# Performance work log

Hardware: AMD Instinct MI355X
Metric: run time of the kernel (lower is better)

Reference implementation:

```python
import jax, jax.numpy as jnp
import numpy as np

N_NODES = 50000
N_RELS = 50
N_CLASSES = 10
EMB = 16
RP = 16
NT = 300000
EPS = 1e-6


def setup_inputs() -> dict:
    key = jax.random.key(0)
    ks = jax.random.split(key, 8)
    # unique (s, o) pairs of the relational graph
    s = jax.random.randint(ks[0], (NT,), 0, N_NODES, dtype=jnp.int32)
    o = jax.random.randint(ks[1], (NT,), 0, N_NODES, dtype=jnp.int32)
    rm = jnp.arange(RP, dtype=jnp.int32)[:, None]  # (rp, 1)
    # hindices = [s, o*rm] in an (n, n*rp) matrix; vindices = [s*rm, o] in (n*rp, n)
    hrow = jnp.broadcast_to(s[None, :], (RP, NT)).reshape(-1)
    hcol = (o[None, :] * rm).reshape(-1)
    vrow = (s[None, :] * rm).reshape(-1)
    vcol = jnp.broadcast_to(o[None, :], (RP, NT)).reshape(-1)
    # nhots: one-hot relation indicator per unique pair
    p = jax.random.randint(ks[2], (NT,), 0, N_RELS)
    nhots = jnp.zeros((NT, N_RELS), jnp.float32).at[jnp.arange(NT), p].set(1.0)
    # to_latent MLPs (ldepth=0 -> single Linear)
    Wl1 = jax.random.normal(ks[3], (N_RELS, RP), jnp.float32) * 0.1
    bl1 = jnp.zeros((RP,), jnp.float32)
    Wl2 = jax.random.normal(ks[4], (N_RELS, RP), jnp.float32) * 0.1
    bl2 = jnp.zeros((RP,), jnp.float32)
    # xavier-uniform-ish init with relu gain
    g1 = np.sqrt(2.0) * np.sqrt(6.0 / (N_NODES + EMB))
    g2 = np.sqrt(2.0) * np.sqrt(6.0 / (EMB + N_CLASSES))
    weights1 = jax.random.uniform(ks[5], (RP, N_NODES, EMB), jnp.float32, -g1, g1)
    weights2 = jax.random.uniform(ks[6], (RP, EMB, N_CLASSES), jnp.float32, -g2, g2)
    bias1 = jnp.zeros((EMB,), jnp.float32)
    bias2 = jnp.zeros((N_CLASSES,), jnp.float32)
    return {
        "nhots": nhots, "hrow": hrow, "hcol": hcol, "vrow": vrow, "vcol": vcol,
        "Wl1": Wl1, "bl1": bl1, "Wl2": Wl2, "bl2": bl2,
        "weights1": weights1, "bias1": bias1, "weights2": weights2, "bias2": bias2,
    }


def reference(nhots, hrow, hcol, vrow, vcol, Wl1, bl1, Wl2, bl2,
              weights1, bias1, weights2, bias2):
    rp, n, e = weights1.shape
    c = weights2.shape[2]
    # --- layer 1: latent relation mixing over horizontal sparse pattern ---
    lat1 = jax.nn.softmax(nhots @ Wl1 + bl1, axis=1)      # (nt, rp)
    lat1 = lat1.T.reshape(-1)                              # (rp*nt,) value per nnz
    # sum_sparse with row=False: normalize by column sums of the (n, n*rp) matrix
    colsum = jax.ops.segment_sum(lat1, hcol, num_segments=n * rp)
    lat1 = lat1 / jnp.clip(colsum[hcol], EPS, None)
    # spmm: (n, n*rp) sparse @ weights1.view(n*rp, e)
    Xw = weights1.reshape(rp * n, e)
    h = jax.ops.segment_sum(lat1[:, None] * Xw[hcol], hrow, num_segments=n)  # (n, e)
    h = jax.nn.relu(h + bias1)
    # --- layer 2: vertical sparse pattern ---
    lat2 = jax.nn.softmax(nhots @ Wl2 + bl2, axis=1)      # (nt, rp)
    lat2 = jax.nn.relu(lat2.T.reshape(-1))                 # LACT = relu
    # sum_sparse with row=True: normalize by row sums of the (n*rp, n) matrix
    rowsum = jax.ops.segment_sum(lat2, vrow, num_segments=n * rp)
    lat2 = lat2 / jnp.clip(rowsum[vrow], EPS, None)
    # spmm: (n*rp, n) sparse @ h
    h2 = jax.ops.segment_sum(lat2[:, None] * h[vcol], vrow, num_segments=n * rp)  # (n*rp, e)
    h2 = h2.reshape(rp, n, e)
    logits = jnp.einsum('rhc,rnh->nc', weights2, h2) + bias2  # (n, c)
    return logits
```

## Files before the change

### kernel.cpp

```cpp
#include <hip/hip_runtime.h>
#include <hip/hip_bf16.h>
#include <stdint.h>

#define NTOT  300000
#define NNODE 50000
#define RPD   16
#define NREL  50
#define EMB   16
#define NC    10
#define EPSF  1e-6f
#define SG    49

typedef const __hip_bfloat16* bf16p;

__device__ __forceinline__ float b2f(__hip_bfloat16 x){ return __bfloat162float(x); }

__device__ __forceinline__ void unpack2(unsigned u, float& a, float& b){
  a = __uint_as_float(u << 16);
  b = __uint_as_float(u & 0xffff0000u);
}

__device__ __forceinline__ float ldf(const void* p, int i, int bf){
  return bf ? b2f(((bf16p)p)[i]) : ((const float*)p)[i];
}

__global__ void k_detect(const unsigned* nraw, int* flag){
  __shared__ int bad;
  if(threadIdx.x == 0) bad = 0;
  __syncthreads();
  for(int i = threadIdx.x; i < 4096; i += 1024){
    unsigned w = nraw[i];
    if(w != 0u && w != 0x3F800000u) bad = 1;
  }
  __syncthreads();
  if(threadIdx.x == 0) *flag = bad;
}

__global__ void k_zero(float* p, long n){
  long i = (long)blockIdx.x*blockDim.x + threadIdx.x;
  long stride = (long)gridDim.x*blockDim.x;
  for(; i < n; i += stride) p[i] = 0.f;
}

__global__ void k_tables(const void* Wl1, const void* bl1, const void* Wl2, const void* bl2,
                         float* T1, float* T2, const int* flag){
  int bf = *flag;
  int i = threadIdx.x;
  const void* W = nullptr; const void* bl = nullptr; float* T = nullptr; int row = -1;
  if(i < NREL){ W = Wl1; bl = bl1; T = T1; row = i; }
  else if(i >= 64 && i < 64 + NREL){ W = Wl2; bl = bl2; T = T2; row = i - 64; }
  if(row >= 0){
    float v[RPD]; float m = -1e30f;
    for(int r = 0; r < RPD; r++){
      v[r] = ldf(W, row*RPD + r, bf) + ldf(bl, r, bf);
      m = fmaxf(m, v[r]);
    }
    float s = 0.f;
    for(int r = 0; r < RPD; r++){ v[r] = __expf(v[r] - m); s += v[r]; }
    float inv = 1.f / s;
    for(int r = 0; r < RPD; r++) T[row*RPD + r] = v[r] * inv;
  }
}

__global__ __launch_bounds__(256) void k_argmax(const void* nhots, const int* srow, const int* ocol,
    int* p, int* cnt_s, int* cnt_o, const int* flag){
  int bf = *flag;
  int t = blockIdx.x*256 + threadIdx.x;
  if(t >= NTOT) return;
  int pt = 0; float best = -1e30f;
  if(bf){
    const unsigned* row = (const unsigned*)nhots + (size_t)t*(NREL/2);
    for(int k = 0; k < NREL/2; k++){
      float a, b; unpack2(row[k], a, b);
      if(a > best){ best = a; pt = 2*k;   }
      if(b > best){ best = b; pt = 2*k+1; }
    }
  } else {
    const uint2* row = (const uint2*)((const float*)nhots + (size_t)t*NREL);
    for(int k = 0; k < NREL/2; k++){
      uint2 u = row[k];
      float a = __uint_as_float(u.x), b = __uint_as_float(u.y);
      if(a > best){ best = a; pt = 2*k;   }
      if(b > best){ best = b; pt = 2*k+1; }
    }
  }
  p[t] = pt;
  atomicAdd(&cnt_s[srow[t]], 1);
  atomicAdd(&cnt_o[ocol[t]], 1);
}

__global__ __launch_bounds__(1024) void k_scanA(const int* cnt_s, const int* cnt_o,
    int* start_s, int* start_o, int* bsum){
  int G = gridDim.x >> 1;
  bool oside = blockIdx.x >= G;
  int b = oside ? blockIdx.x - G : blockIdx.x;
  const int* cnt = oside ? cnt_o : cnt_s;
  int* start = oside ? start_o : start_s;
  __shared__ int sh[1024];
  int tid = threadIdx.x;
  int idx = b*1024 + tid;
  int v = (idx < NNODE) ? cnt[idx] : 0;
  sh[tid] = v;
  __syncthreads();
  for(int off = 1; off < 1024; off <<= 1){
    int n = (tid >= off) ? sh[tid - off] : 0;
    __syncthreads();
    sh[tid] += n;
    __syncthreads();
  }
  if(idx < NNODE) start[idx] = sh[tid] - v;
  if(tid == 1023) bsum[(oside ? G : 0) + b] = sh[1023];
}

__global__ void k_scanB(int* bsum, int* start_s, int* start_o){
  int tid = threadIdx.x;
  bool oside = tid >= 64;
  int lane = tid & 63;
  int base = oside ? SG : 0;
  int v = (lane < SG) ? bsum[base + lane] : 0;
  int orig = v;
  for(int off = 1; off < 64; off <<= 1){
    int n = __shfl_up(v, off);
    if(lane >= off) v += n;
  }
  if(lane < SG) bsum[base + lane] = v - orig;
  if(lane == 63){
    if(oside) start_o[NNODE] = v; else start_s[NNODE] = v;
  }
}

__global__ __launch_bounds__(1024) void k_scanC(int* start_s, int* start_o,
    int* cursor_s, int* cursor_o, const int* bsum){
  int G = gridDim.x >> 1;
  bool oside = blockIdx.x >= G;
  int b = oside ? blockIdx.x - G : blockIdx.x;
  int idx = b*1024 + threadIdx.x;
  if(idx >= NNODE) return;
  int ofs = bsum[(oside ? G : 0) + b];
  int* start  = oside ? start_o  : start_s;
  int* cursor = oside ? cursor_o : cursor_s;
  int v = start[idx] + ofs;
  start[idx] = v;
  cursor[idx] = v;
}

__global__ void k_fill2(const int* srow, const int* ocol, int* cursor_s, int* cursor_o,
                        int* eidx_s, int* pos_s, int* eidx_o){
  int half = gridDim.x >> 1;
  bool oside = blockIdx.x >= half;
  int b = oside ? blockIdx.x - half : blockIdx.x;
  int t = b*256 + threadIdx.x;
  if(t >= NTOT) return;
  if(oside){ int pos = atomicAdd(&cursor_o[ocol[t]], 1); eidx_o[pos] = t; }
  else     { int pos = atomicAdd(&cursor_s[srow[t]], 1); eidx_s[pos] = t; pos_s[t] = pos; }
}

__global__ __launch_bounds__(256) void k_S12(const int* start_s, const int* eidx_s,
    const int* start_o, const int* eidx_o, const int* p, const float* T1, const float* T2,
    float* S1, float* S2, float* floodS){
  int G = gridDim.x >> 1;
  bool oside = blockIdx.x >= G;
  int b = oside ? blockIdx.x - G : blockIdx.x;
  const int* start = oside ? start_o : start_s;
  const int* eidx  = oside ? eidx_o  : eidx_s;
  const float* T   = oside ? T1 : T2;
  float* S         = oside ? S1 : S2;
  __shared__ float lT[NREL*RPD];
  __shared__ float w0[4];
  int tid = threadIdx.x;
  for(int i = tid; i < NREL*RPD; i += 256) lT[i] = T[i];
  __syncthreads();
  int wave = tid >> 6, lane = tid & 63;
  int r = lane & 15, quarter = lane >> 4;
  float flood = 0.f;
  for(int node = b*4 + wave; node < NNODE; node += G*4){
    float acc = 0.f;
    int e0 = start[node], e1 = start[node+1];
    for(int e = e0 + quarter; e < e1; e += 4)
      acc += lT[p[eidx[e]]*RPD + r];
    acc += __shfl_xor(acc, 16);
    acc += __shfl_xor(acc, 32);
    if(quarter == 0){
      S[node*RPD + r] = acc;
      if(r == 0) flood += acc;
    }
  }
  if(lane == 0) w0[wave] = flood;
  __syncthreads();
  if(tid == 0)
    atomicAdd(&floodS[(oside ? 0 : 64) + (b & 63)], w0[0]+w0[1]+w0[2]+w0[3]);
}

__global__ __launch_bounds__(256) void k_icolsum(const float* S1, const float* floodS, float* icolsum){
  int stride = gridDim.x*256;
  for(int v = blockIdx.x*256 + threadIdx.x; v < NNODE*RPD; v += stride){
    float acc = 0.f;
    #pragma unroll
    for(int r = 1; r <= 15; r++){
      if(v % (unsigned)r == 0u){
        int s = (unsigned)v / (unsigned)r;
        if(s < NNODE) acc += S1[s*RPD + r];
      }
    }
    if(v == 0){
      float f = 0.f;
      for(int k = 0; k < 64; k++) f += floodS[k];
      acc += f;
    }
    icolsum[v] = 1.f / fmaxf(acc, EPSF);
  }
}

__global__ __launch_bounds__(256) void k_hC(const int* eidx_o, const int* ocol,
    const int* pos_s, const int* p, const float* T1, const float* icolsum,
    const void* W1, float* C, const int* flag){
  __shared__ float lT1[NREL*RPD];
  int bf = *flag;
  int tid = threadIdx.x;
  for(int i = tid; i < NREL*RPD; i += 256) lT1[i] = T1[i];
  __syncthreads();
  int id = blockIdx.x*256 + tid;
  int e = id >> 2, q = id & 3;
  if(e >= NTOT) return;
  int t  = eidx_o[e];
  int o  = ocol[t];
  int pt = p[t];
  int ps = pos_s[t];
  const float* t1 = lT1 + pt*RPD;
  float4 acc = {0.f,0.f,0.f,0.f};
  #pragma unroll
  for(int r = 0; r < RPD; r++){
    int c = o * r;
    float w = t1[r] * icolsum[c];
    float4 f;
    if(bf){
      uint2 u = *((const uint2*)((const char*)W1 + (size_t)c*32) + q);
      unpack2(u.x, f.x, f.y); unpack2(u.y, f.z, f.w);
    } else {
      f = ((const float4*)W1)[(size_t)c*4 + q];
    }
    acc.x += w*f.x; acc.y += w*f.y; acc.z += w*f.z; acc.w += w*f.w;
  }
  ((float4*)C)[(size_t)ps*4 + q] = acc;
}

__global__ void k_hsum(const int* start_s, const float* C, const void* bias1,
                       float* h, const int* flag){
  int bf = *flag;
  int id = blockIdx.x*256 + threadIdx.x;
  if(id >= NNODE*4) return;
  int s = id >> 2, q = id & 3;
  int e0 = start_s[s], e1 = start_s[s+1];
  float4 acc = {0.f,0.f,0.f,0.f};
  for(int e = e0; e < e1; e++){
    float4 c = ((const float4*)C)[(size_t)e*4 + q];
    acc.x += c.x; acc.y += c.y; acc.z += c.z; acc.w += c.w;
  }
  float4 o4;
  o4.x = fmaxf(acc.x + ldf(bias1, q*4+0, bf), 0.f);
  o4.y = fmaxf(acc.y + ldf(bias1, q*4+1, bf), 0.f);
  o4.z = fmaxf(acc.z + ldf(bias1, q*4+2, bf), 0.f);
  o4.w = fmaxf(acc.w + ldf(bias1, q*4+3, bf), 0.f);
  ((float4*)h)[(size_t)s*4 + q] = o4;
}

__global__ __launch_bounds__(256) void k_E(const int* start_s, const int* eidx_s,
    const int* ocol, const int* p, const float* T2, const float* h,
    float* E, float* floodE){
  __shared__ float lT2[NREL*RPD];
  __shared__ float sred[4][16];
  int tid = threadIdx.x;
  for(int i = tid; i < NREL*RPD; i += 256) lT2[i] = T2[i];
  __syncthreads();
  int wave = tid >> 6, lane = tid & 63;
  int r = lane >> 2, q = lane & 3;
  float4 fl = {0.f,0.f,0.f,0.f};
  int wstride = gridDim.x*4;
  for(int s = blockIdx.x*4 + wave; s < NNODE; s += wstride){
    float4 Ev = {0.f,0.f,0.f,0.f};
    int e0 = start_s[s], e1 = start_s[s+1];
    for(int e = e0; e < e1; e++){
      int t = eidx_s[e];
      int o = ocol[t];
      float sc = lT2[p[t]*RPD + r];
      float4 hf = ((const float4*)h)[(size_t)o*4 + q];
      Ev.x += sc*hf.x; Ev.y += sc*hf.y; Ev.z += sc*hf.z; Ev.w += sc*hf.w;
    }
    ((float4*)E)[(size_t)s*64 + lane] = Ev;
    if(r == 0){ fl.x += Ev.x; fl.y += Ev.y; fl.z += Ev.z; fl.w += Ev.w; }
  }
  if(r == 0){
    sred[wave][q*4+0] = fl.x; sred[wave][q*4+1] = fl.y;
    sred[wave][q*4+2] = fl.z; sred[wave][q*4+3] = fl.w;
  }
  __syncthreads();
  if(tid < 16){
    float v = sred[0][tid]+sred[1][tid]+sred[2][tid]+sred[3][tid];
    atomicAdd(&floodE[(blockIdx.x & 63)*16 + tid], v);
  }
}

__global__ __launch_bounds__(256) void k_logitsB(const float* E, const float* S2,
    const void* W2, const void* bias2, const float* floodS, const float* floodE,
    void* out, const int* flag){
  __shared__ float lW2[15*EMB*NC];
  int bf = *flag;
  int tid = threadIdx.x;
  for(int i = tid; i < 15*EMB*NC; i += 256) lW2[i] = ldf(W2, i, bf);
  __syncthreads();
  int npi = blockIdx.x*256 + tid;
  if(npi >= NNODE) return;
  float acc[NC];
  #pragma unroll
  for(int c = 0; c < NC; c++) acc[c] = ldf(bias2, c, bf);
  #pragma unroll 1
  for(int rpi = 0; rpi < 15; rpi++){
    unsigned v = (unsigned)rpi*NNODE + (unsigned)npi;
    float4 ea = {0.f,0.f,0.f,0.f}, eb = ea, ec = ea, ed = ea;
    float rsum = 0.f;
    #pragma unroll
    for(int r = 1; r <= 15; r++){
      if(v % (unsigned)r == 0u){
        unsigned s = v / (unsigned)r;
        if(s < NNODE){
          rsum += S2[s*RPD + r];
          const float4* Ep = (const float4*)(E + (size_t)s*256 + r*16);
          float4 a = Ep[0], b = Ep[1], c4 = Ep[2], d = Ep[3];
          ea.x += a.x; ea.y += a.y; ea.z += a.z; ea.w += a.w;
          eb.x += b.x; eb.y += b.y; eb.z += b.z; eb.w += b.w;
          ec.x += c4.x; ec.y += c4.y; ec.z += c4.z; ec.w += c4.w;
          ed.x += d.x; ed.y += d.y; ed.z += d.z; ed.w += d.w;
        }
      }
    }
    if(rpi == 0 && npi == 0){
      for(int k = 0; k < 64; k++) rsum += floodS[64 + k];
      for(int k = 0; k < 64; k++){
        const float* fE = floodE + k*16;
        ea.x += fE[0];  ea.y += fE[1];  ea.z += fE[2];  ea.w += fE[3];
        eb.x += fE[4];  eb.y += fE[5];  eb.z += fE[6];  eb.w += fE[7];
        ec.x += fE[8];  ec.y += fE[9];  ec.z += fE[10]; ec.w += fE[11];
        ed.x += fE[12]; ed.y += fE[13]; ed.z += fE[14]; ed.w += fE[15];
      }
    }
    float inv = 1.f / fmaxf(rsum, EPSF);
    const float* w2 = lW2 + rpi*EMB*NC;
    #pragma unroll
    for(int c = 0; c < NC; c++){
      float g = w2[0*NC+c]*ea.x  + w2[1*NC+c]*ea.y  + w2[2*NC+c]*ea.z  + w2[3*NC+c]*ea.w
              + w2[4*NC+c]*eb.x  + w2[5*NC+c]*eb.y  + w2[6*NC+c]*eb.z  + w2[7*NC+c]*eb.w
              + w2[8*NC+c]*ec.x  + w2[9*NC+c]*ec.y  + w2[10*NC+c]*ec.z + w2[11*NC+c]*ec.w
              + w2[12*NC+c]*ed.x + w2[13*NC+c]*ed.y + w2[14*NC+c]*ed.z + w2[15*NC+c]*ed.w;
      acc[c] += inv * g;
    }
  }
  if(bf){
    #pragma unroll
    for(int c = 0; c < NC; c++) ((__hip_bfloat16*)out)[(size_t)npi*NC + c] = __float2bfloat16(acc[c]);
  } else {
    #pragma unroll
    for(int c = 0; c < NC; c++) ((float*)out)[(size_t)npi*NC + c] = acc[c];
  }
}

extern "C" void kernel_launch(void* const* d_in, const int* in_sizes, int n_in,
                              void* d_out, int out_size, void* d_ws, size_t ws_size,
                              hipStream_t stream){
  const void* nhots = d_in[0];
  const int* hrow = (const int*)d_in[1];
  const int* vcol = (const int*)d_in[4];
  const void* Wl1 = d_in[5];
  const void* bl1 = d_in[6];
  const void* Wl2 = d_in[7];
  const void* bl2 = d_in[8];
  const void* W1  = d_in[9];
  const void* bias1 = d_in[10];
  const void* W2  = d_in[11];
  const void* bias2 = d_in[12];

  float* ws = (float*)d_ws;
  int*   flag    = (int*)ws;
  float* T1      = ws + 16;
  float* T2      = T1 + 800;
  int*   p       = (int*)(T2 + 800);
  int*   start_s = p + 300000;
  int*   start_o = start_s + 50004;
  int*   eidx_s  = start_o + 50004;
  int*   pos_s   = eidx_s + 300000;
  int*   eidx_o  = pos_s + 300000;
  float* S2      = (float*)(eidx_o + 300000);
  float* h       = S2 + 800000;
  int*   cnt_s   = (int*)(h + 800000);
  int*   cnt_o   = cnt_s + 50000;
  float* floodS  = (float*)(cnt_o + 50000);
  float* floodE  = floodS + 128;
  int*   cursor_s= (int*)(floodE + 1024);
  int*   cursor_o= cursor_s + 50000;
  int*   bsum    = cursor_o + 50000;
  float* A       = (float*)(bsum + 128);
  float* S1      = A;
  float* icolsum = A + 800000;
  float* C       = A + 1600000;
  float* E       = A;

  k_detect<<<1, 1024, 0, stream>>>((const unsigned*)nhots, flag);
  k_zero<<<396, 256, 0, stream>>>((float*)cnt_s, 101152L);
  k_tables<<<1, 128, 0, stream>>>(Wl1, bl1, Wl2, bl2, T1, T2, flag);

  const int nblk = (NTOT + 255) / 256;
  k_argmax<<<nblk, 256, 0, stream>>>(nhots, hrow, vcol, p, cnt_s, cnt_o, flag);
  k_scanA<<<2*SG, 1024, 0, stream>>>(cnt_s, cnt_o, start_s, start_o, bsum);
  k_scanB<<<1, 128, 0, stream>>>(bsum, start_s, start_o);
  k_scanC<<<2*SG, 1024, 0, stream>>>(start_s, start_o, cursor_s, cursor_o, bsum);
  k_fill2<<<2*nblk, 256, 0, stream>>>(hrow, vcol, cursor_s, cursor_o, eidx_s, pos_s, eidx_o);
  k_S12<<<25000, 256, 0, stream>>>(start_s, eidx_s, start_o, eidx_o, p, T1, T2, S1, S2, floodS);
  k_icolsum<<<1024, 256, 0, stream>>>(S1, floodS, icolsum);
  k_hC<<<(NTOT*4 + 255)/256, 256, 0, stream>>>(eidx_o, vcol, pos_s, p, T1, icolsum, W1, C, flag);
  k_hsum<<<(NNODE*4 + 255)/256, 256, 0, stream>>>(start_s, C, bias1, h, flag);
  k_E<<<6250, 256, 0, stream>>>(start_s, eidx_s, vcol, p, T2, h, E, floodE);
  k_logitsB<<<(NNODE + 255)/256, 256, 0, stream>>>(E, S2, W2, bias2, floodS, floodE, d_out, flag);
}
```

Baseline: 512.1 us.

## Pack edge records in CSR fill and fuse S2 row sums into k_E

The fill kernel now writes packed per-edge records (target node, relation id and s-side position) straight into the CSR order of both sides, replacing the eidx/pos_s indirection chains. Downstream kernels read one record instead of chasing eidx→ocol/p/pos_s. The S2 row sums are computed inside k_E, so the combined S12 kernel becomes an o-side-only S1 kernel, and the per-node kernels launch one block per four nodes instead of using grid-stride loops. Packing depends on node ids fitting in 16 bits (50000 does), positions in 19 bits and relation ids in the remaining bits.

```diff
diff --git a/kernel.cpp b/kernel.cpp
--- a/kernel.cpp
+++ b/kernel.cpp
@@ -144,54 +144,46 @@
   cursor[idx] = v;
 }
 
-__global__ void k_fill2(const int* srow, const int* ocol, int* cursor_s, int* cursor_o,
-                        int* eidx_s, int* pos_s, int* eidx_o){
-  int half = gridDim.x >> 1;
-  bool oside = blockIdx.x >= half;
-  int b = oside ? blockIdx.x - half : blockIdx.x;
-  int t = b*256 + threadIdx.x;
+__global__ void k_fill(const int* srow, const int* ocol, const int* p,
+                       int* cursor_s, int* cursor_o, int* rec_s, int2* rec_o){
+  int t = blockIdx.x*256 + threadIdx.x;
   if(t >= NTOT) return;
-  if(oside){ int pos = atomicAdd(&cursor_o[ocol[t]], 1); eidx_o[pos] = t; }
-  else     { int pos = atomicAdd(&cursor_s[srow[t]], 1); eidx_s[pos] = t; pos_s[t] = pos; }
-}
-
-__global__ __launch_bounds__(256) void k_S12(const int* start_s, const int* eidx_s,
-    const int* start_o, const int* eidx_o, const int* p, const float* T1, const float* T2,
-    float* S1, float* S2, float* floodS){
-  int G = gridDim.x >> 1;
-  bool oside = blockIdx.x >= G;
-  int b = oside ? blockIdx.x - G : blockIdx.x;
-  const int* start = oside ? start_o : start_s;
-  const int* eidx  = oside ? eidx_o  : eidx_s;
-  const float* T   = oside ? T1 : T2;
-  float* S         = oside ? S1 : S2;
+  int s = srow[t], o = ocol[t], pt = p[t];
+  int pos  = atomicAdd(&cursor_s[s], 1);
+  int posO = atomicAdd(&cursor_o[o], 1);
+  rec_s[pos] = o | (pt << 16);
+  int2 r; r.x = pos | (pt << 19); r.y = o;
+  rec_o[posO] = r;
+}
+
+__global__ __launch_bounds__(256) void k_S1(const int* start_o, const int2* rec_o,
+    const float* T1, float* S1, float* floodSo){
   __shared__ float lT[NREL*RPD];
   __shared__ float w0[4];
   int tid = threadIdx.x;
-  for(int i = tid; i < NREL*RPD; i += 256) lT[i] = T[i];
+  for(int i = tid; i < NREL*RPD; i += 256) lT[i] = T1[i];
   __syncthreads();
   int wave = tid >> 6, lane = tid & 63;
   int r = lane & 15, quarter = lane >> 4;
-  float flood = 0.f;
-  for(int node = b*4 + wave; node < NNODE; node += G*4){
-    float acc = 0.f;
-    int e0 = start[node], e1 = start[node+1];
-    for(int e = e0 + quarter; e < e1; e += 4)
-      acc += lT[p[eidx[e]]*RPD + r];
-    acc += __shfl_xor(acc, 16);
-    acc += __shfl_xor(acc, 32);
-    if(quarter == 0){
-      S[node*RPD + r] = acc;
-      if(r == 0) flood += acc;
-    }
-  }
-  if(lane == 0) w0[wave] = flood;
+  int node = blockIdx.x*4 + wave;
+  float acc = 0.f;
+  int e0 = start_o[node], e1 = start_o[node+1];
+  for(int e = e0 + quarter; e < e1; e += 4){
+    int pt = ((unsigned)rec_o[e].x) >> 19;
+    acc += lT[pt*RPD + r];
+  }
+  acc += __shfl_xor(acc, 16);
+  acc += __shfl_xor(acc, 32);
+  if(quarter == 0){
+    S1[node*RPD + r] = acc;
+  }
+  if(lane == 0) w0[wave] = acc;
   __syncthreads();
   if(tid == 0)
-    atomicAdd(&floodS[(oside ? 0 : 64) + (b & 63)], w0[0]+w0[1]+w0[2]+w0[3]);
-}
-
-__global__ __launch_bounds__(256) void k_icolsum(const float* S1, const float* floodS, float* icolsum){
+    atomicAdd(&floodSo[blockIdx.x & 63], w0[0]+w0[1]+w0[2]+w0[3]);
+}
+
+__global__ __launch_bounds__(256) void k_icolsum(const float* S1, const float* floodSo, float* icolsum){
   int stride = gridDim.x*256;
   for(int v = blockIdx.x*256 + threadIdx.x; v < NNODE*RPD; v += stride){
     float acc = 0.f;
@@ -204,16 +196,15 @@
     }
     if(v == 0){
       float f = 0.f;
-      for(int k = 0; k < 64; k++) f += floodS[k];
+      for(int k = 0; k < 64; k++) f += floodSo[k];
       acc += f;
     }
     icolsum[v] = 1.f / fmaxf(acc, EPSF);
   }
 }
 
-__global__ __launch_bounds__(256) void k_hC(const int* eidx_o, const int* ocol,
-    const int* pos_s, const int* p, const float* T1, const float* icolsum,
-    const void* W1, float* C, const int* flag){
+__global__ __launch_bounds__(256) void k_hC(const int2* rec_o, const float* T1,
+    const float* icolsum, const void* W1, float* C, const int* flag){
   __shared__ float lT1[NREL*RPD];
   int bf = *flag;
   int tid = threadIdx.x;
@@ -222,10 +213,10 @@
   int id = blockIdx.x*256 + tid;
   int e = id >> 2, q = id & 3;
   if(e >= NTOT) return;
-  int t  = eidx_o[e];
-  int o  = ocol[t];
-  int pt = p[t];
-  int ps = pos_s[t];
+  int2 rec = rec_o[e];
+  int psx = rec.x & 0x7FFFF;
+  int pt  = ((unsigned)rec.x) >> 19;
+  int o   = rec.y;
   const float* t1 = lT1 + pt*RPD;
   float4 acc = {0.f,0.f,0.f,0.f};
   #pragma unroll
@@ -241,7 +232,7 @@
     }
     acc.x += w*f.x; acc.y += w*f.y; acc.z += w*f.z; acc.w += w*f.w;
   }
-  ((float4*)C)[(size_t)ps*4 + q] = acc;
+  ((float4*)C)[(size_t)psx*4 + q] = acc;
 }
 
 __global__ void k_hsum(const int* start_s, const float* C, const void* bias1,
@@ -264,44 +255,48 @@
   ((float4*)h)[(size_t)s*4 + q] = o4;
 }
 
-__global__ __launch_bounds__(256) void k_E(const int* start_s, const int* eidx_s,
-    const int* ocol, const int* p, const float* T2, const float* h,
-    float* E, float* floodE){
+__global__ __launch_bounds__(256) void k_E(const int* start_s, const int* rec_s,
+    const float* T2, const float* h, float* E, float* S2,
+    float* floodE, float* floodS2){
   __shared__ float lT2[NREL*RPD];
   __shared__ float sred[4][16];
+  __shared__ float sred2[4];
   int tid = threadIdx.x;
   for(int i = tid; i < NREL*RPD; i += 256) lT2[i] = T2[i];
   __syncthreads();
   int wave = tid >> 6, lane = tid & 63;
   int r = lane >> 2, q = lane & 3;
-  float4 fl = {0.f,0.f,0.f,0.f};
-  int wstride = gridDim.x*4;
-  for(int s = blockIdx.x*4 + wave; s < NNODE; s += wstride){
-    float4 Ev = {0.f,0.f,0.f,0.f};
-    int e0 = start_s[s], e1 = start_s[s+1];
-    for(int e = e0; e < e1; e++){
-      int t = eidx_s[e];
-      int o = ocol[t];
-      float sc = lT2[p[t]*RPD + r];
-      float4 hf = ((const float4*)h)[(size_t)o*4 + q];
-      Ev.x += sc*hf.x; Ev.y += sc*hf.y; Ev.z += sc*hf.z; Ev.w += sc*hf.w;
-    }
-    ((float4*)E)[(size_t)s*64 + lane] = Ev;
-    if(r == 0){ fl.x += Ev.x; fl.y += Ev.y; fl.z += Ev.z; fl.w += Ev.w; }
-  }
+  int s = blockIdx.x*4 + wave;
+  float4 Ev = {0.f,0.f,0.f,0.f};
+  float scs = 0.f;
+  int e0 = start_s[s], e1 = start_s[s+1];
+  for(int e = e0; e < e1; e++){
+    int w = rec_s[e];
+    int o = w & 0xFFFF;
+    int pt = ((unsigned)w) >> 16;
+    float sc = lT2[pt*RPD + r];
+    float4 hf = ((const float4*)h)[(size_t)o*4 + q];
+    Ev.x += sc*hf.x; Ev.y += sc*hf.y; Ev.z += sc*hf.z; Ev.w += sc*hf.w;
+    scs += sc;
+  }
+  ((float4*)E)[(size_t)s*64 + lane] = Ev;
+  if(q == 0) S2[s*RPD + r] = scs;
   if(r == 0){
-    sred[wave][q*4+0] = fl.x; sred[wave][q*4+1] = fl.y;
-    sred[wave][q*4+2] = fl.z; sred[wave][q*4+3] = fl.w;
+    sred[wave][q*4+0] = Ev.x; sred[wave][q*4+1] = Ev.y;
+    sred[wave][q*4+2] = Ev.z; sred[wave][q*4+3] = Ev.w;
+    if(q == 0) sred2[wave] = scs;
   }
   __syncthreads();
   if(tid < 16){
     float v = sred[0][tid]+sred[1][tid]+sred[2][tid]+sred[3][tid];
     atomicAdd(&floodE[(blockIdx.x & 63)*16 + tid], v);
   }
+  if(tid == 0)
+    atomicAdd(&floodS2[blockIdx.x & 63], sred2[0]+sred2[1]+sred2[2]+sred2[3]);
 }
 
 __global__ __launch_bounds__(256) void k_logitsB(const float* E, const float* S2,
-    const void* W2, const void* bias2, const float* floodS, const float* floodE,
+    const void* W2, const void* bias2, const float* floodS2, const float* floodE,
     void* out, const int* flag){
   __shared__ float lW2[15*EMB*NC];
   int bf = *flag;
@@ -334,7 +329,7 @@
       }
     }
     if(rpi == 0 && npi == 0){
-      for(int k = 0; k < 64; k++) rsum += floodS[64 + k];
+      for(int k = 0; k < 64; k++) rsum += floodS2[k];
       for(int k = 0; k < 64; k++){
         const float* fE = floodE + k*16;
         ea.x += fE[0];  ea.y += fE[1];  ea.z += fE[2];  ea.w += fE[3];
@@ -383,24 +378,24 @@
   float* T1      = ws + 16;
   float* T2      = T1 + 800;
   int*   p       = (int*)(T2 + 800);
-  int*   start_s = p + 300000;
+  int*   rec_s   = p + 300000;
+  int*   start_s = rec_s + 300000;
   int*   start_o = start_s + 50004;
-  int*   eidx_s  = start_o + 50004;
-  int*   pos_s   = eidx_s + 300000;
-  int*   eidx_o  = pos_s + 300000;
-  float* S2      = (float*)(eidx_o + 300000);
-  float* h       = S2 + 800000;
-  int*   cnt_s   = (int*)(h + 800000);
-  int*   cnt_o   = cnt_s + 50000;
-  float* floodS  = (float*)(cnt_o + 50000);
-  float* floodE  = floodS + 128;
-  int*   cursor_s= (int*)(floodE + 1024);
+  int*   cursor_s= start_o + 50004;
   int*   cursor_o= cursor_s + 50000;
   int*   bsum    = cursor_o + 50000;
-  float* A       = (float*)(bsum + 128);
+  int*   cnt_s   = bsum + 128;
+  int*   cnt_o   = cnt_s + 50000;
+  float* floodSo = (float*)(cnt_o + 50000);
+  float* floodS2 = floodSo + 64;
+  float* floodE  = floodS2 + 64;
+  float* S2      = floodE + 1024;
+  float* h       = S2 + 800000;
+  float* A       = h + 800000;
   float* S1      = A;
   float* icolsum = A + 800000;
   float* C       = A + 1600000;
+  int2*  rec_o   = (int2*)(A + 6400000);
   float* E       = A;
 
   k_detect<<<1, 1024, 0, stream>>>((const unsigned*)nhots, flag);
@@ -412,11 +407,11 @@
   k_scanA<<<2*SG, 1024, 0, stream>>>(cnt_s, cnt_o, start_s, start_o, bsum);
   k_scanB<<<1, 128, 0, stream>>>(bsum, start_s, start_o);
   k_scanC<<<2*SG, 1024, 0, stream>>>(start_s, start_o, cursor_s, cursor_o, bsum);
-  k_fill2<<<2*nblk, 256, 0, stream>>>(hrow, vcol, cursor_s, cursor_o, eidx_s, pos_s, eidx_o);
-  k_S12<<<25000, 256, 0, stream>>>(start_s, eidx_s, start_o, eidx_o, p, T1, T2, S1, S2, floodS);
-  k_icolsum<<<1024, 256, 0, stream>>>(S1, floodS, icolsum);
-  k_hC<<<(NTOT*4 + 255)/256, 256, 0, stream>>>(eidx_o, vcol, pos_s, p, T1, icolsum, W1, C, flag);
+  k_fill<<<nblk, 256, 0, stream>>>(hrow, vcol, p, cursor_s, cursor_o, rec_s, rec_o);
+  k_S1<<<12500, 256, 0, stream>>>(start_o, rec_o, T1, S1, floodSo);
+  k_icolsum<<<1024, 256, 0, stream>>>(S1, floodSo, icolsum);
+  k_hC<<<(NTOT*4 + 255)/256, 256, 0, stream>>>(rec_o, T1, icolsum, W1, C, flag);
   k_hsum<<<(NNODE*4 + 255)/256, 256, 0, stream>>>(start_s, C, bias1, h, flag);
-  k_E<<<6250, 256, 0, stream>>>(start_s, eidx_s, vcol, p, T2, h, E, floodE);
-  k_logitsB<<<(NNODE + 255)/256, 256, 0, stream>>>(E, S2, W2, bias2, floodS, floodE, d_out, flag);
-}
+  k_E<<<12500, 256, 0, stream>>>(start_s, rec_s, T2, h, E, S2, floodE, floodS2);
+  k_logitsB<<<(NNODE + 255)/256, 256, 0, stream>>>(E, S2, W2, bias2, floodS2, floodE, d_out, flag);
+}
```

After: 501.0 us. -2.2%, faster.
